# Kernel tuning notes

Measured on AMD Instinct MI355X. Metric: run time of the kernel, lower is better.

## Reference

```python
import jax, jax.numpy as jnp
import numpy as np

L = 8192   # residues / nodes
E = 524288 # contact-map edges (avg degree 64)
NEG_SLOPE = 0.2  # PyG GATConv default negative_slope


def gat_layer(x, src, dst, Wg, asrc, adst, bias):
    """PyG-style GATConv (v1), concat heads, eval mode (no dropout).
    x: [L, F_in]; Wg: [F_in, H*C]; asrc/adst: [H, C]; bias: [H*C]."""
    H, C = asrc.shape
    h = (x @ Wg).reshape(L, H, C)                      # [L,H,C]
    a_s = jnp.einsum('nhc,hc->nh', h, asrc)            # [L,H]
    a_d = jnp.einsum('nhc,hc->nh', h, adst)            # [L,H]
    e = jax.nn.leaky_relu(a_s[src] + a_d[dst], NEG_SLOPE)  # [E',H]
    # softmax over incoming edges of each destination node
    m = jax.ops.segment_max(e, dst, num_segments=L)
    ex = jnp.exp(e - m[dst])
    denom = jax.ops.segment_sum(ex, dst, num_segments=L)
    alpha = ex / (denom[dst] + 1e-16)                  # [E',H]
    msg = h[src] * alpha[:, :, None]                   # [E',H,C]
    out = jax.ops.segment_sum(msg, dst, num_segments=L)  # [L,H,C]
    return out.reshape(L, H * C) + bias


def setup_inputs() -> dict:
    key = jax.random.key(0)
    ks = jax.random.split(key, 16)
    def g(k, shape, scale=0.05):
        return (jax.random.normal(k, shape, dtype=jnp.float32) * scale)
    return {
        'input_seq': jax.random.normal(ks[0], (1, L, 26), dtype=jnp.float32),
        'edge_index': jax.random.randint(ks[1], (2, E), 0, L, dtype=jnp.int32),
        'W1': g(ks[2], (26, 1024)),
        'W2': g(ks[3], (1024, 256)),
        'Wg1': g(ks[4], (256, 256)),
        'asrc1': g(ks[5], (4, 64)),
        'adst1': g(ks[6], (4, 64)),
        'b1': g(ks[7], (256,)),
        'Wg2': g(ks[8], (256, 512)),
        'asrc2': g(ks[9], (4, 128)),
        'adst2': g(ks[10], (4, 128)),
        'b2': g(ks[11], (512,)),
        'fcW': g(ks[12], (512, 512)),
        'fcb': g(ks[13], (512,)),
        'outW': g(ks[14], (512, 489)),
        'outb': g(ks[15], (489,)),
    }


def reference(input_seq, edge_index, W1, W2, Wg1, asrc1, adst1, b1,
              Wg2, asrc2, adst2, b2, fcW, fcb, outW, outb):
    # input_layer: Linear(26,1024,no bias) -> ReLU -> Linear(1024,256,no bias)
    x = jax.nn.relu(input_seq[0] @ W1) @ W2            # [L,256]
    # add self-loops (PyG GATConv default)
    loops = jnp.arange(L, dtype=edge_index.dtype)
    src = jnp.concatenate([edge_index[0], loops])
    dst = jnp.concatenate([edge_index[1], loops])
    # two GAT layers with ReLU activation
    x = jax.nn.relu(gat_layer(x, src, dst, Wg1, asrc1, adst1, b1))  # [L,256]
    x = jax.nn.relu(gat_layer(x, src, dst, Wg2, asrc2, adst2, b2))  # [L,512]
    # sum-pool over residues (x.sum(dim=1) with batch=1)
    pooled = x.sum(axis=0, keepdims=True)              # [1,512]
    # fc layers (dropout inactive in eval)
    h = jax.nn.relu(pooled @ fcW + fcb)                # [1,512]
    return h @ outW + outb                             # [1,489]
```

## Files before the change

### kernel.cpp

```cpp
#include <hip/hip_runtime.h>
#include <hip/hip_bf16.h>

constexpr int L = 8192;
constexpr int H = 4;

typedef __attribute__((ext_vector_type(8))) short bf16x8;
typedef __attribute__((ext_vector_type(8))) unsigned short u16x8;
typedef __attribute__((ext_vector_type(4))) float f32x4;

#if defined(__has_builtin)
#  if __has_builtin(__builtin_amdgcn_fdot2_f32_bf16)
#    define HAVE_DOT2 1
#  endif
#endif
#ifndef HAVE_DOT2
#  define HAVE_DOT2 0
#endif
#if HAVE_DOT2
typedef __attribute__((ext_vector_type(2))) __bf16 bfx2;
#endif

static __device__ __forceinline__ float lrelu(float e) {
  return e > 0.f ? e : 0.2f * e;
}
static __device__ __forceinline__ float b2f(unsigned short s) {
  return __uint_as_float(((unsigned)s) << 16);
}
static __device__ __forceinline__ unsigned short f2b(float f) {
  __hip_bfloat16 h = __float2bfloat16(f);
  return *reinterpret_cast<unsigned short*>(&h);
}

template<int PAIRS>
static __device__ __forceinline__ void edge_fma(const unsigned* hv, uint2 m, float* acc) {
#if HAVE_DOT2
#pragma unroll
  for (int p = 0; p < PAIRS; p++) {
    acc[2 * p]     = __builtin_amdgcn_fdot2_f32_bf16(
        __builtin_bit_cast(bfx2, hv[p]), __builtin_bit_cast(bfx2, m.x), acc[2 * p], false);
    acc[2 * p + 1] = __builtin_amdgcn_fdot2_f32_bf16(
        __builtin_bit_cast(bfx2, hv[p]), __builtin_bit_cast(bfx2, m.y), acc[2 * p + 1], false);
  }
#else
  float af = b2f((unsigned short)(m.x & 0xffffu));
#pragma unroll
  for (int p = 0; p < PAIRS; p++) {
    acc[2 * p]     = fmaf(af, b2f((unsigned short)(hv[p] & 0xffffu)), acc[2 * p]);
    acc[2 * p + 1] = fmaf(af, b2f((unsigned short)(hv[p] >> 16)), acc[2 * p + 1]);
  }
#endif
}

__global__ __launch_bounds__(256) void conv_combo(
    const float* __restrict__ seq, const float* __restrict__ W1,
    const float* __restrict__ W2, const float* __restrict__ Wg1,
    const float* __restrict__ Wg2, const float* __restrict__ fcW,
    const float* __restrict__ outW, const int* __restrict__ ei,
    const float* __restrict__ as1, const float* __restrict__ ad1,
    const float* __restrict__ as2, const float* __restrict__ ad2,
    int E, int Etot,
    __hip_bfloat16* __restrict__ xb, __hip_bfloat16* __restrict__ W1t,
    __hip_bfloat16* __restrict__ W2t, __hip_bfloat16* __restrict__ Wg1t,
    __hip_bfloat16* __restrict__ Wg2t, float* __restrict__ fcWt,
    float* __restrict__ outWt, float* __restrict__ wa2,
    int* __restrict__ deg, int* __restrict__ rank) {
  __shared__ float tile[32][33];
  if (blockIdx.x < 992) {
    int b = blockIdx.x;
    const float* src; void* dst; bool obf16; int K, N, Kout, kt, nt;
    if (b < 256)               { src = W2;  dst = W2t;  obf16 = true;  K = 1024; N = 256; Kout = 1024; nt = b & 7;  kt = b >> 3; }
    else if ((b -= 256) < 64)  { src = Wg1; dst = Wg1t; obf16 = true;  K = 256;  N = 256; Kout = 256;  nt = b & 7;  kt = b >> 3; }
    else if ((b -= 64) < 128)  { src = Wg2; dst = Wg2t; obf16 = true;  K = 256;  N = 512; Kout = 256;  nt = b & 15; kt = b >> 4; }
    else if ((b -= 128) < 256) { src = fcW; dst = fcWt; obf16 = false; K = 512;  N = 512; Kout = 512;  nt = b & 15; kt = b >> 4; }
    else if ((b -= 256) < 256) { src = outW;dst = outWt;obf16 = false; K = 512;  N = 489; Kout = 512;  nt = b & 15; kt = b >> 4; }
    else { b -= 256;             src = W1;  dst = W1t;  obf16 = true;  K = 26;   N = 1024;Kout = 32;   nt = b;      kt = 0; }
    int t = threadIdx.x;
    int lr = t >> 3, lc4 = (t & 7) * 4;
    int gk = kt * 32 + lr, gn = nt * 32 + lc4;
    float4 v = {0.f, 0.f, 0.f, 0.f};
    if (gk < K) {
      const float* p = &src[(size_t)gk * N + gn];
      v.x = (gn + 0 < N) ? p[0] : 0.f;
      v.y = (gn + 1 < N) ? p[1] : 0.f;
      v.z = (gn + 2 < N) ? p[2] : 0.f;
      v.w = (gn + 3 < N) ? p[3] : 0.f;
    }
    tile[lr][lc4 + 0] = v.x; tile[lr][lc4 + 1] = v.y;
    tile[lr][lc4 + 2] = v.z; tile[lr][lc4 + 3] = v.w;
    __syncthreads();
    int on = nt * 32 + lr, ok = kt * 32 + lc4;
    if (on >= N || ok >= Kout) return;
    float o0 = tile[lc4 + 0][lr], o1 = tile[lc4 + 1][lr];
    float o2 = tile[lc4 + 2][lr], o3 = tile[lc4 + 3][lr];
    if (obf16) {
      ushort4 u = {f2b(o0), f2b(o1), f2b(o2), f2b(o3)};
      *(ushort4*)&((__hip_bfloat16*)dst)[(size_t)on * Kout + ok] = u;
    } else {
      float4 u = {o0, o1, o2, o3};
      *(float4*)&((float*)dst)[(size_t)on * Kout + ok] = u;
    }
    return;
  }
  int i = (blockIdx.x - 992) * 256 + threadIdx.x;
  if (i < 262144) { int r = i >> 5, k = i & 31;
    xb[i] = __float2bfloat16(k < 26 ? seq[r * 26 + k] : 0.f); return; }
  i -= 262144;
  if (i < 2048) {
    int k = i >> 3, o = i & 7, h = o & 3;
    const float* av = (o < 4) ? as1 : ad1;
    float s = 0.f;
    for (int c = 0; c < 64; c++) s += Wg1[k * 256 + h * 64 + c] * av[h * 64 + c];
    Wg1t[(size_t)(256 + o) * 256 + k] = __float2bfloat16(s); return; }
  i -= 2048;
  if (i < 2048) {
    int k = i >> 3, o = i & 7, h = o & 3;
    const float* av = (o < 4) ? as2 : ad2;
    float s = 0.f;
    for (int c = 0; c < 128; c++) s += Wg2[k * 512 + h * 128 + c] * av[h * 128 + c];
    wa2[i] = s; return; }
  i -= 2048;
  if (i < 14336) {
    ((__hip_bfloat16*)Wg1t)[(size_t)264 * 256 + i] = __float2bfloat16(0.f); return; }
  i -= 14336;
  if (i < Etot) {
    int dst = (i < E) ? ei[E + i] : (i - E);
    rank[i] = atomicAdd(&deg[dst], 1);
  }
}

template<int BK, bool RELU, bool ASD>
__global__ __launch_bounds__(256) void gemm_big(
    const __hip_bfloat16* __restrict__ A, const __hip_bfloat16* __restrict__ Bt,
    __hip_bfloat16* __restrict__ C, float* __restrict__ asd,
    int M, int N, int K) {
  __shared__ __align__(16) short As[128][BK + 8];
  __shared__ __align__(16) short Bs[64][BK + 8];
  int tid = threadIdx.x;
  int m0 = blockIdx.y * 128, n0 = blockIdx.x * 64;
  int w = tid >> 6, lane = tid & 63;
  int wm = (w >> 1) * 64, wn = (w & 1) * 32;
  f32x4 acc[4][2] = {};
  for (int k0 = 0; k0 < K; k0 += BK) {
    if constexpr (BK == 64) {
#pragma unroll
      for (int i = 0; i < 4; i++) {
        int ch = i * 256 + tid; int r = ch >> 3, kg = ch & 7;
        *(bf16x8*)&As[r][kg * 8] = *(const bf16x8*)&A[(size_t)(m0 + r) * K + k0 + kg * 8];
      }
#pragma unroll
      for (int i = 0; i < 2; i++) {
        int ch = i * 256 + tid; int r = ch >> 3, kg = ch & 7;
        *(bf16x8*)&Bs[r][kg * 8] = *(const bf16x8*)&Bt[(size_t)(n0 + r) * K + k0 + kg * 8];
      }
    } else {
#pragma unroll
      for (int i = 0; i < 2; i++) {
        int ch = i * 256 + tid; int r = ch >> 2, kg = ch & 3;
        *(bf16x8*)&As[r][kg * 8] = *(const bf16x8*)&A[(size_t)(m0 + r) * K + k0 + kg * 8];
      }
      { int r = tid >> 2, kg = tid & 3;
        *(bf16x8*)&Bs[r][kg * 8] = *(const bf16x8*)&Bt[(size_t)(n0 + r) * K + k0 + kg * 8]; }
    }
    __syncthreads();
    int kk = (lane >> 4) * 8;
#pragma unroll
    for (int ks = 0; ks < BK / 32; ks++) {
      bf16x8 af[4], bfr[2];
#pragma unroll
      for (int m = 0; m < 4; m++)
        af[m] = *(const bf16x8*)&As[wm + m * 16 + (lane & 15)][ks * 32 + kk];
#pragma unroll
      for (int n = 0; n < 2; n++)
        bfr[n] = *(const bf16x8*)&Bs[wn + n * 16 + (lane & 15)][ks * 32 + kk];
#pragma unroll
      for (int m = 0; m < 4; m++)
#pragma unroll
        for (int n = 0; n < 2; n++)
          acc[m][n] = __builtin_amdgcn_mfma_f32_16x16x32_bf16(af[m], bfr[n], acc[m][n], 0, 0, 0);
    }
    __syncthreads();
  }
#pragma unroll
  for (int m = 0; m < 4; m++) {
#pragma unroll
    for (int n = 0; n < 2; n++) {
      int col = n0 + wn + n * 16 + (lane & 15);
#pragma unroll
      for (int j = 0; j < 4; j++) {
        int row = m0 + wm + m * 16 + (lane >> 4) * 4 + j;
        float v = acc[m][n][j];
        if (RELU) v = fmaxf(v, 0.f);
        if (!ASD) {
          C[(size_t)row * N + col] = __float2bfloat16(v);
        } else {
          if (col < N) C[(size_t)row * N + col] = __float2bfloat16(v);
          else if (col < N + 8) asd[(size_t)row * 8 + (col - N)] = v;
        }
      }
    }
  }
}

__global__ __launch_bounds__(1024) void scan_deg(const int* __restrict__ deg,
                                                 int* __restrict__ row_start,
                                                 float* __restrict__ pooled) {
  __shared__ int wsum[16];
  int t = threadIdx.x;
  if (t < 512) pooled[t] = 0.f;
  int lane = t & 63, w = t >> 6;
  int local[8];
  int sum = 0;
#pragma unroll
  for (int j = 0; j < 8; j++) { local[j] = deg[t * 8 + j]; sum += local[j]; }
  int v = sum;
#pragma unroll
  for (int off = 1; off < 64; off <<= 1) {
    int u = __shfl_up(v, off);
    if (lane >= off) v += u;
  }
  if (lane == 63) wsum[w] = v;
  __syncthreads();
  int woff = 0;
  for (int i = 0; i < w; i++) woff += wsum[i];
  int base = woff + v - sum;
#pragma unroll
  for (int j = 0; j < 8; j++) { row_start[t * 8 + j] = base; base += local[j]; }
  if (t == 1023) row_start[L] = base;
}

__global__ void scatter_edges(const int* __restrict__ ei, int E, int Etot,
                              const int* __restrict__ row_start,
                              const int* __restrict__ rank, int* __restrict__ csr_src) {
  int e = blockIdx.x * blockDim.x + threadIdx.x;
  if (e >= Etot) return;
  int srcv, dstv;
  if (e < E) { srcv = ei[e]; dstv = ei[E + e]; } else { srcv = dstv = e - E; }
  csr_src[row_start[dstv] + rank[e]] = srcv;
}

template<int C, bool ASD2>
__global__ __launch_bounds__(128) void gat_fused(
    const __hip_bfloat16* __restrict__ hfeat, const float* __restrict__ a_sd,
    const int* __restrict__ row_start, const int* __restrict__ csr_src,
    const float* __restrict__ bias, __hip_bfloat16* __restrict__ out,
    const float* __restrict__ wa2, float* __restrict__ a_sd2) {
  constexpr int HC = 4 * C;
  constexpr int VEC = HC / 64;
  constexpr int PAIRS = VEC / 2;
  constexpr int BATCH = 8;
  int wid = threadIdx.x >> 6, lane = threadIdx.x & 63;
  int n = blockIdx.x * 2 + wid;
  int c0 = lane * VEC;
  int hh = lane >> 4;
  int rs = row_start[n], re = row_start[n + 1];
  float4 ad4 = *(const float4*)&a_sd[(size_t)n * 8 + 4];

  __shared__ __align__(16) uint2 s_m[2][64][4];
  float dp[4] = {0.f, 0.f, 0.f, 0.f};
  float acc[VEC] = {};
  const unsigned short* hbase = (const unsigned short*)hfeat;

  int base = rs;
  int cnt = min(64, re - rs);
  int srcv = 0;
  float4 as4 = {0.f, 0.f, 0.f, 0.f};
  if (lane < cnt) {
    srcv = csr_src[rs + lane];
    as4 = *(const float4*)&a_sd[(size_t)srcv * 8];
  }

  while (base < re) {
    float w0 = 0.f, w1 = 0.f, w2 = 0.f, w3 = 0.f;
    if (lane < cnt) {
      w0 = __expf(lrelu(as4.x + ad4.x));
      w1 = __expf(lrelu(as4.y + ad4.y));
      w2 = __expf(lrelu(as4.z + ad4.z));
      w3 = __expf(lrelu(as4.w + ad4.w));
    }
    dp[0] += w0; dp[1] += w1; dp[2] += w2; dp[3] += w3;
    unsigned l0 = f2b(w0), l1 = f2b(w1), l2 = f2b(w2), l3 = f2b(w3);
    uint4 ma = {l0, l0 << 16, l1, l1 << 16};
    uint4 mb = {l2, l2 << 16, l3, l3 << 16};
    *(uint4*)&s_m[wid][lane][0] = ma;
    *(uint4*)&s_m[wid][lane][2] = mb;
    asm volatile("s_waitcnt lgkmcnt(0)" ::: "memory");
    int cur_src = srcv;
    int cur_cnt = cnt;
    int nbase = base + 64;
    bool have_next = nbase < re;
    cnt = min(64, re - nbase);
    srcv = 0;
    if (have_next && lane < cnt) srcv = csr_src[nbase + lane];
    float4 nas4 = {0.f, 0.f, 0.f, 0.f};
    bool did_asd = false;

    int j = 0;
    for (; j + BATCH <= cur_cnt; j += BATCH) {
      int srs[BATCH];
#pragma unroll
      for (int k = 0; k < BATCH; k++) srs[k] = __builtin_amdgcn_readlane(cur_src, j + k);
      unsigned hv[BATCH][PAIRS];
#pragma unroll
      for (int k = 0; k < BATCH; k++) {
        const unsigned short* hp = &hbase[(size_t)srs[k] * HC + c0];
        if constexpr (PAIRS == 4) *(uint4*)&hv[k][0] = *(const uint4*)hp;
        else                      *(uint2*)&hv[k][0] = *(const uint2*)hp;
      }
      if (j == 0 && have_next) {
        if (lane < cnt) nas4 = *(const float4*)&a_sd[(size_t)srcv * 8];
        did_asd = true;
      }
#pragma unroll
      for (int k = 0; k < BATCH; k++) {
        uint2 m = s_m[wid][j + k][hh];
        edge_fma<PAIRS>(hv[k], m, acc);
      }
    }
    if (have_next && !did_asd && lane < cnt)
      nas4 = *(const float4*)&a_sd[(size_t)srcv * 8];
    for (; j < cur_cnt; j++) {
      int sr = __builtin_amdgcn_readlane(cur_src, j);
      unsigned hv[PAIRS];
      const unsigned short* hp = &hbase[(size_t)sr * HC + c0];
      if constexpr (PAIRS == 4) *(uint4*)&hv[0] = *(const uint4*)hp;
      else                      *(uint2*)&hv[0] = *(const uint2*)hp;
      uint2 m = s_m[wid][j][hh];
      edge_fma<PAIRS>(hv, m, acc);
    }
    as4 = nas4;
    base = nbase;
  }

#pragma unroll
  for (int off = 32; off > 0; off >>= 1) {
#pragma unroll
    for (int h = 0; h < 4; h++) dp[h] += __shfl_xor(dp[h], off);
  }
  float dsel = hh == 0 ? dp[0] : hh == 1 ? dp[1] : hh == 2 ? dp[2] : dp[3];
  float inv = 1.f / (dsel + 1e-16f);

#pragma unroll
  for (int k = 0; k < VEC; k++)
    acc[k] = fmaxf(fmaf(acc[k], inv, bias[c0 + k]), 0.f);
  unsigned short* op = (unsigned short*)out + (size_t)n * HC + c0;
  if constexpr (VEC == 8) {
    u16x8 ov;
#pragma unroll
    for (int k = 0; k < 8; k++) ov[k] = f2b(acc[k]);
    *(u16x8*)op = ov;
  } else {
    ushort4 ov = {f2b(acc[0]), f2b(acc[1]), f2b(acc[2]), f2b(acc[3])};
    *(ushort4*)op = ov;
  }

  if constexpr (ASD2) {
    float p[8] = {};
#pragma unroll
    for (int q = 0; q < VEC; q++) {
      const float* wr = &wa2[(size_t)(c0 + q) * 8];
#pragma unroll
      for (int o = 0; o < 8; o++) p[o] = fmaf(acc[q], wr[o], p[o]);
    }
#pragma unroll
    for (int off = 32; off > 0; off >>= 1) {
#pragma unroll
      for (int o = 0; o < 8; o++) p[o] += __shfl_xor(p[o], off);
    }
    if (lane == 0) {
      float4 p0 = {p[0], p[1], p[2], p[3]};
      float4 p1 = {p[4], p[5], p[6], p[7]};
      *(float4*)&a_sd2[(size_t)n * 8 + 0] = p0;
      *(float4*)&a_sd2[(size_t)n * 8 + 4] = p1;
    }
  }
}

__global__ __launch_bounds__(512) void col_sum_bf16(const __hip_bfloat16* __restrict__ x,
                                                    float* __restrict__ pooled) {
  int t = threadIdx.x;
  float acc = 0.f;
  for (int r = blockIdx.x; r < L; r += 64)
    acc += b2f(*(const unsigned short*)&x[(size_t)r * 512 + t]);
  atomicAdd(&pooled[t], acc);
}

__global__ __launch_bounds__(256) void fc1(const float* __restrict__ pooled,
                                           const float* __restrict__ Wt,
                                           const float* __restrict__ b,
                                           float* __restrict__ out) {
  __shared__ float pv[512];
  __shared__ float red[256];
  int t = threadIdx.x;
  pv[t] = pooled[t]; pv[t + 256] = pooled[t + 256];
  __syncthreads();
  int ol = t >> 4;
  int o = blockIdx.x * 16 + ol;
  int ks = (t & 15) * 32;
  float p = 0.f;
  const float* wr = &Wt[(size_t)o * 512 + ks];
#pragma unroll
  for (int kk = 0; kk < 32; kk++) p = fmaf(pv[ks + kk], wr[kk], p);
  red[t] = p;
  __syncthreads();
  if ((t & 15) == 0) {
    float s2 = 0.f;
#pragma unroll
    for (int i = 0; i < 16; i++) s2 += red[ol * 16 + i];
    out[o] = fmaxf(s2 + b[o], 0.f);
  }
}

__global__ __launch_bounds__(256) void fc2(const float* __restrict__ h,
                                           const float* __restrict__ Wt,
                                           const float* __restrict__ outb,
                                           float* __restrict__ out) {
  __shared__ float pv[512];
  __shared__ float red[256];
  int t = threadIdx.x;
  pv[t] = h[t]; pv[t + 256] = h[t + 256];
  __syncthreads();
  int ol = t >> 4;
  int o = blockIdx.x * 16 + ol;
  int ks = (t & 15) * 32;
  float p = 0.f;
  const float* wr = &Wt[(size_t)o * 512 + ks];
#pragma unroll
  for (int kk = 0; kk < 32; kk++) p = fmaf(pv[ks + kk], wr[kk], p);
  red[t] = p;
  __syncthreads();
  if ((t & 15) == 0 && o < 489) {
    float s2 = 0.f;
#pragma unroll
    for (int i = 0; i < 16; i++) s2 += red[ol * 16 + i];
    out[o] = s2 + outb[o];
  }
}

extern "C" void kernel_launch(void* const* d_in, const int* in_sizes, int n_in,
                              void* d_out, int out_size, void* d_ws, size_t ws_size,
                              hipStream_t stream) {
  const float* seq   = (const float*)d_in[0];
  const int*   ei    = (const int*)d_in[1];
  const float* W1    = (const float*)d_in[2];
  const float* W2    = (const float*)d_in[3];
  const float* Wg1   = (const float*)d_in[4];
  const float* asrc1 = (const float*)d_in[5];
  const float* adst1 = (const float*)d_in[6];
  const float* b1    = (const float*)d_in[7];
  const float* Wg2   = (const float*)d_in[8];
  const float* asrc2 = (const float*)d_in[9];
  const float* adst2 = (const float*)d_in[10];
  const float* b2    = (const float*)d_in[11];
  const float* fcW   = (const float*)d_in[12];
  const float* fcb   = (const float*)d_in[13];
  const float* outW  = (const float*)d_in[14];
  const float* outb  = (const float*)d_in[15];
  float* outp = (float*)d_out;

  const int E = in_sizes[1] / 2;
  const int Etot = E + L;

  char* ws = (char*)d_ws;
  __hip_bfloat16* mlp1 = (__hip_bfloat16*)(ws + 0);
  __hip_bfloat16* out2 = (__hip_bfloat16*)(ws + 0);
  __hip_bfloat16* h2   = (__hip_bfloat16*)(ws + (16u << 20));
  __hip_bfloat16* x0   = (__hip_bfloat16*)(ws + (24u << 20));
  __hip_bfloat16* h1   = (__hip_bfloat16*)(ws + (28u << 20));
  __hip_bfloat16* out1 = (__hip_bfloat16*)(ws + (32u << 20));
  size_t off = (36u << 20);
  __hip_bfloat16* xb   = (__hip_bfloat16*)(ws + off); off += (size_t)L * 32 * 2;
  __hip_bfloat16* W1t  = (__hip_bfloat16*)(ws + off); off += (size_t)1024 * 32 * 2;
  __hip_bfloat16* W2t  = (__hip_bfloat16*)(ws + off); off += (size_t)256 * 1024 * 2;
  __hip_bfloat16* Wg1t = (__hip_bfloat16*)(ws + off); off += (size_t)320 * 256 * 2;
  __hip_bfloat16* Wg2t = (__hip_bfloat16*)(ws + off); off += (size_t)512 * 256 * 2;
  float* fcWt  = (float*)(ws + off); off += (size_t)512 * 512 * 4;
  float* outWt = (float*)(ws + off); off += (size_t)512 * 512 * 4;
  int* csr_src = (int*)(ws + off); off += (size_t)Etot * 4;
  int* rank    = (int*)(ws + off); off += (size_t)Etot * 4;
  off = (off + 255) & ~(size_t)255;
  int* row_start = (int*)(ws + off); off += (size_t)(L + 1) * 4;
  off = (off + 255) & ~(size_t)255;
  int* deg    = (int*)(ws + off); off += (size_t)L * 4;
  float* a_sd1 = (float*)(ws + off); off += (size_t)L * 8 * 4;
  float* a_sd2 = (float*)(ws + off); off += (size_t)L * 8 * 4;
  float* wa2 = (float*)(ws + off); off += 2048 * 4;
  float* pooled = (float*)(ws + off); off += 512 * 4;
  float* hbuf   = (float*)(ws + off); off += 512 * 4;

  hipMemsetAsync(deg, 0, (size_t)L * 4, stream);

  int convN = 262144 + 2048 + 2048 + 14336 + Etot;
  int convB = (convN + 255) / 256;
  conv_combo<<<992 + convB, 256, 0, stream>>>(
      seq, W1, W2, Wg1, Wg2, fcW, outW, ei, asrc1, adst1, asrc2, adst2, E, Etot,
      xb, W1t, W2t, Wg1t, Wg2t, fcWt, outWt, wa2, deg, rank);

  scan_deg<<<1, 1024, 0, stream>>>(deg, row_start, pooled);
  scatter_edges<<<(Etot + 255) / 256, 256, 0, stream>>>(ei, E, Etot, row_start, rank, csr_src);

  gemm_big<32, true, false><<<dim3(16, 64), 256, 0, stream>>>(xb, W1t, mlp1, nullptr, L, 1024, 32);
  gemm_big<64, false, false><<<dim3(4, 64), 256, 0, stream>>>(mlp1, W2t, x0, nullptr, L, 256, 1024);

  gemm_big<64, false, true><<<dim3(5, 64), 256, 0, stream>>>(x0, Wg1t, h1, a_sd1, L, 256, 256);
  gat_fused<64, true><<<4096, 128, 0, stream>>>(h1, a_sd1, row_start, csr_src, b1, out1, wa2, a_sd2);

  gemm_big<64, false, false><<<dim3(8, 64), 256, 0, stream>>>(out1, Wg2t, h2, nullptr, L, 512, 256);
  gat_fused<128, false><<<4096, 128, 0, stream>>>(h2, a_sd2, row_start, csr_src, b2, out2, nullptr, nullptr);

  col_sum_bf16<<<64, 512, 0, stream>>>(out2, pooled);
  fc1<<<32, 256, 0, stream>>>(pooled, fcWt, fcb, hbuf);
  fc2<<<31, 256, 0, stream>>>(hbuf, outWt, outb, outp);
}
```

Measured before the change: 221.7 us.

## Split layer-2 GAT aggregation across two column-phase blocks and widen batch

```diff
diff --git a/kernel.cpp b/kernel.cpp
--- a/kernel.cpp
+++ b/kernel.cpp
@@ -238,20 +238,21 @@
   csr_src[row_start[dstv] + rank[e]] = srcv;
 }
 
-template<int C, bool ASD2>
+template<int C, int PHASES, bool ASD2>
 __global__ __launch_bounds__(128) void gat_fused(
     const __hip_bfloat16* __restrict__ hfeat, const float* __restrict__ a_sd,
     const int* __restrict__ row_start, const int* __restrict__ csr_src,
     const float* __restrict__ bias, __hip_bfloat16* __restrict__ out,
     const float* __restrict__ wa2, float* __restrict__ a_sd2) {
   constexpr int HC = 4 * C;
-  constexpr int VEC = HC / 64;
+  constexpr int VEC = HC / PHASES / 64;
   constexpr int PAIRS = VEC / 2;
-  constexpr int BATCH = 8;
+  constexpr int BATCH = 12;
   int wid = threadIdx.x >> 6, lane = threadIdx.x & 63;
   int n = blockIdx.x * 2 + wid;
-  int c0 = lane * VEC;
-  int hh = lane >> 4;
+  int c0 = blockIdx.y * 256 + lane * VEC;
+  int hh = c0 / C;
+  int hl = hh & 3;
   int rs = row_start[n], re = row_start[n + 1];
   float4 ad4 = *(const float4*)&a_sd[(size_t)n * 8 + 4];
 
@@ -303,8 +304,7 @@
 #pragma unroll
       for (int k = 0; k < BATCH; k++) {
         const unsigned short* hp = &hbase[(size_t)srs[k] * HC + c0];
-        if constexpr (PAIRS == 4) *(uint4*)&hv[k][0] = *(const uint4*)hp;
-        else                      *(uint2*)&hv[k][0] = *(const uint2*)hp;
+        *(uint2*)&hv[k][0] = *(const uint2*)hp;
       }
       if (j == 0 && have_next) {
         if (lane < cnt) nas4 = *(const float4*)&a_sd[(size_t)srcv * 8];
@@ -312,7 +312,7 @@
       }
 #pragma unroll
       for (int k = 0; k < BATCH; k++) {
-        uint2 m = s_m[wid][j + k][hh];
+        uint2 m = s_m[wid][j + k][hl];
         edge_fma<PAIRS>(hv[k], m, acc);
       }
     }
@@ -322,9 +322,8 @@
       int sr = __builtin_amdgcn_readlane(cur_src, j);
       unsigned hv[PAIRS];
       const unsigned short* hp = &hbase[(size_t)sr * HC + c0];
-      if constexpr (PAIRS == 4) *(uint4*)&hv[0] = *(const uint4*)hp;
-      else                      *(uint2*)&hv[0] = *(const uint2*)hp;
-      uint2 m = s_m[wid][j][hh];
+      *(uint2*)&hv[0] = *(const uint2*)hp;
+      uint2 m = s_m[wid][j][hl];
       edge_fma<PAIRS>(hv, m, acc);
     }
     as4 = nas4;
@@ -336,22 +335,15 @@
 #pragma unroll
     for (int h = 0; h < 4; h++) dp[h] += __shfl_xor(dp[h], off);
   }
-  float dsel = hh == 0 ? dp[0] : hh == 1 ? dp[1] : hh == 2 ? dp[2] : dp[3];
+  float dsel = hl == 0 ? dp[0] : hl == 1 ? dp[1] : hl == 2 ? dp[2] : dp[3];
   float inv = 1.f / (dsel + 1e-16f);
 
 #pragma unroll
   for (int k = 0; k < VEC; k++)
     acc[k] = fmaxf(fmaf(acc[k], inv, bias[c0 + k]), 0.f);
   unsigned short* op = (unsigned short*)out + (size_t)n * HC + c0;
-  if constexpr (VEC == 8) {
-    u16x8 ov;
-#pragma unroll
-    for (int k = 0; k < 8; k++) ov[k] = f2b(acc[k]);
-    *(u16x8*)op = ov;
-  } else {
-    ushort4 ov = {f2b(acc[0]), f2b(acc[1]), f2b(acc[2]), f2b(acc[3])};
-    *(ushort4*)op = ov;
-  }
+  ushort4 ov = {f2b(acc[0]), f2b(acc[1]), f2b(acc[2]), f2b(acc[3])};
+  *(ushort4*)op = ov;
 
   if constexpr (ASD2) {
     float p[8] = {};
@@ -502,10 +494,10 @@
   gemm_big<64, false, false><<<dim3(4, 64), 256, 0, stream>>>(mlp1, W2t, x0, nullptr, L, 256, 1024);
 
   gemm_big<64, false, true><<<dim3(5, 64), 256, 0, stream>>>(x0, Wg1t, h1, a_sd1, L, 256, 256);
-  gat_fused<64, true><<<4096, 128, 0, stream>>>(h1, a_sd1, row_start, csr_src, b1, out1, wa2, a_sd2);
+  gat_fused<64, 1, true><<<dim3(4096, 1), 128, 0, stream>>>(h1, a_sd1, row_start, csr_src, b1, out1, wa2, a_sd2);
 
   gemm_big<64, false, false><<<dim3(8, 64), 256, 0, stream>>>(out1, Wg2t, h2, nullptr, L, 512, 256);
-  gat_fused<128, false><<<4096, 128, 0, stream>>>(h2, a_sd2, row_start, csr_src, b2, out2, nullptr, nullptr);
+  gat_fused<128, 2, false><<<dim3(4096, 2), 128, 0, stream>>>(h2, a_sd2, row_start, csr_src, b2, out2, nullptr, nullptr);
 
   col_sum_bf16<<<64, 512, 0, stream>>>(out2, pooled);
   fc1<<<32, 256, 0, stream>>>(pooled, fcWt, fcb, hbuf);
```

Result: no change. 220.5 us (-0.5%).
